# Optimization experiments

Measured on AMD Instinct MI355X. Metric: run time of the kernel, lower is better.

Reference implementation:

```python
import jax, jax.numpy as jnp
import numpy as np


def _patch_indices():
    # 36 positions (6x6 grid), each gathering a 3x3 window of 6-channel squares
    # from the flattened 385-vector: index = x*48 + y*6 + c
    idx = []
    for i in range(36):
        x, y = i // 6, i % 6
        rows = []
        for ox in range(3):
            for oy in range(3):
                base = (x + ox) * 48 + (y + oy) * 6
                rows.extend(range(base, base + 6))
        idx.append(rows)
    return jnp.asarray(np.array(idx, dtype=np.int32))  # [36, 54]


_IDX = _patch_indices()


def _crelu(v):
    return jnp.clip(v, -1.0, 1.0)


def setup_inputs() -> dict:
    key = jax.random.key(0)
    ks = jax.random.split(key, 13)
    B = 131072
    inp = jax.random.normal(ks[0], (B, 385), dtype=jnp.float32)
    s = 0.2  # small init scale
    # sight stack: 54 -> 8 -> 8 -> 1  (stored as [in, out])
    W1 = jax.random.normal(ks[1], (54, 8), jnp.float32) * s
    b1 = jax.random.normal(ks[2], (8,), jnp.float32) * s
    W2 = jax.random.normal(ks[3], (8, 8), jnp.float32) * s
    b2 = jax.random.normal(ks[4], (8,), jnp.float32) * s
    W3 = jax.random.normal(ks[5], (8, 1), jnp.float32) * s
    b3 = jax.random.normal(ks[6], (1,), jnp.float32) * s
    # evaluation stack: 37 -> 16 -> 16 -> 1
    E1 = jax.random.normal(ks[7], (37, 16), jnp.float32) * s
    c1 = jax.random.normal(ks[8], (16,), jnp.float32) * s
    E2 = jax.random.normal(ks[9], (16, 16), jnp.float32) * s
    c2 = jax.random.normal(ks[10], (16,), jnp.float32) * s
    E3 = jax.random.normal(ks[11], (16, 1), jnp.float32) * s
    c3 = jax.random.normal(ks[12], (1,), jnp.float32) * s
    return {"inp": inp, "W1": W1, "b1": b1, "W2": W2, "b2": b2,
            "W3": W3, "b3": b3, "E1": E1, "c1": c1, "E2": E2, "c2": c2,
            "E3": E3, "c3": c3}


def reference(inp, W1, b1, W2, b2, W3, b3, E1, c1, E2, c2, E3, c3):
    # inp: [B, 385]
    patches = inp[:, _IDX]                       # [B, 36, 54] windowed gather
    h = _crelu(jnp.einsum('bpf,fo->bpo', patches, W1) + b1)   # [B, 36, 8]
    h = _crelu(jnp.einsum('bpf,fo->bpo', h, W2) + b2)         # [B, 36, 8]
    v = _crelu(jnp.einsum('bpf,fo->bpo', h, W3) + b3)[..., 0]  # [B, 36]
    vision = jnp.concatenate([v, inp[:, 384:385]], axis=1)    # [B, 37]
    g = _crelu(vision @ E1 + c1)                 # [B, 16]
    g = _crelu(g @ E2 + c2)                      # [B, 16]
    out = _crelu(g @ E3 + c3)                    # [B, 1]
    return out
```

## Files before the change

kernel.cpp:

```cpp
#include <hip/hip_runtime.h>

typedef __attribute__((ext_vector_type(8))) short short8;
typedef __attribute__((ext_vector_type(4))) float float4v;

__device__ __forceinline__ float crelu(float v) {
    return fminf(1.0f, fmaxf(-1.0f, v));
}
__device__ __forceinline__ ushort f2bf(float v) {
    uint u = __float_as_uint(v);
    u += 0x7fffu + ((u >> 16) & 1u);
    return (ushort)(u >> 16);
}

#define ROW 385
#define BT 16
#define BS 388
#define BOARD_ELEMS (BT * BS)
#define BOARD_TOTAL (BOARD_ELEMS + 64)

__global__ __launch_bounds__(256, 6)
void lila_mfma(const float* __restrict__ inp,
               const float* __restrict__ W1, const float* __restrict__ b1,
               const float* __restrict__ W2, const float* __restrict__ b2,
               const float* __restrict__ W3, const float* __restrict__ b3,
               const float* __restrict__ E1, const float* __restrict__ c1,
               const float* __restrict__ E2, const float* __restrict__ c2,
               const float* __restrict__ E3, const float* __restrict__ c3,
               float* __restrict__ out)
{
    __shared__ __align__(16) ushort s_board[BOARD_TOTAL];
    __shared__ __align__(16) ushort s_h[BT * 36 * 8];
    __shared__ float s_vis[BT * 37];
    __shared__ float s_cen[BT];
    __shared__ float s_g1[BT * 17];
    __shared__ float s_g2[BT * 17];

    const int tid  = threadIdx.x;
    const int lane = tid & 63;
    const int wv   = tid >> 6;
    const int quad = lane >> 4;
    const int nn   = tid & 15;
    const int m0   = quad * 8;
    const long long b0 = (long long)blockIdx.x * BT;

    short8 bfr[3];
    #pragma unroll
    for (int r = 0; r < 3; ++r) {
        #pragma unroll
        for (int j = 0; j < 8; ++j) {
            int k = m0 + j;
            float w = (k < 18 && nn < 8) ? W1[(r * 18 + k) * 8 + nn] : 0.0f;
            bfr[r][j] = (short)f2bf(w);
        }
    }
    const float bias1 = (nn < 8) ? b1[nn] : 0.0f;

    #pragma unroll 1
    for (int rr = 0; rr < 4; ++rr) {
        int row = wv * 4 + rr;
        const float* gr = inp + (b0 + row) * ROW;
        ushort* br = s_board + row * BS;
        #pragma unroll
        for (int s = 0; s < 6; ++s)
            br[lane + 64 * s] = f2bf(gr[lane + 64 * s]);
        if (lane == 0) s_cen[row] = gr[384];
        if (lane < 4)  br[384 + lane] = 0;
    }
    if (tid < 64) s_board[BOARD_ELEMS + tid] = 0;
    __syncthreads();

    #pragma unroll 1
    for (int t = wv; t < 36; t += 4) {
        int task = t * 16 + nn;
        uint b = (uint)task / 36u;
        uint p = (uint)task - 36u * b;
        uint x = p / 6u;
        uint y = p - 6u * x;
        const uint* bp = (const uint*)(s_board + b * BS + x * 48 + 6 * y + m0);
        union { uint u[4]; short8 s; } a0, a1, a2;
        #pragma unroll
        for (int q = 0; q < 4; ++q) {
            a0.u[q] = bp[q];
            a1.u[q] = bp[24 + q];
            a2.u[q] = bp[48 + q];
        }
        float4v acc = { bias1, bias1, bias1, bias1 };
        acc = __builtin_amdgcn_mfma_f32_16x16x32_bf16(a0.s, bfr[0], acc, 0, 0, 0);
        acc = __builtin_amdgcn_mfma_f32_16x16x32_bf16(a1.s, bfr[1], acc, 0, 0, 0);
        acc = __builtin_amdgcn_mfma_f32_16x16x32_bf16(a2.s, bfr[2], acc, 0, 0, 0);
        if (nn < 8) {
            #pragma unroll
            for (int i = 0; i < 4; ++i) {
                int trow = t * 16 + quad * 4 + i;
                s_h[trow * 8 + nn] = f2bf(crelu(acc[i]));
            }
        }
    }
    __syncthreads();

    #pragma unroll 1
    for (int task = tid; task < BT * 36; task += 256) {
        uint b = (uint)task / 36u;
        uint p = (uint)task - 36u * b;
        const uint4* hp = (const uint4*)s_h;
        uint4 hv = hp[task];
        float h[8];
        h[0] = __uint_as_float(hv.x << 16);
        h[1] = __uint_as_float(hv.x & 0xffff0000u);
        h[2] = __uint_as_float(hv.y << 16);
        h[3] = __uint_as_float(hv.y & 0xffff0000u);
        h[4] = __uint_as_float(hv.z << 16);
        h[5] = __uint_as_float(hv.z & 0xffff0000u);
        h[6] = __uint_as_float(hv.w << 16);
        h[7] = __uint_as_float(hv.w & 0xffff0000u);

        float a2[8];
        #pragma unroll
        for (int o = 0; o < 8; ++o) a2[o] = b2[o];
        #pragma unroll
        for (int i = 0; i < 8; ++i) {
            #pragma unroll
            for (int o = 0; o < 8; ++o)
                a2[o] = fmaf(h[i], W2[i * 8 + o], a2[o]);
        }
        float v = b3[0];
        #pragma unroll
        for (int i = 0; i < 8; ++i) v = fmaf(crelu(a2[i]), W3[i], v);
        s_vis[b * 37 + p] = crelu(v);
    }
    if (tid < BT) s_vis[tid * 37 + 36] = s_cen[tid];
    __syncthreads();

    {
        int b = tid & 15, o = tid >> 4;
        float a = c1[o];
        #pragma unroll
        for (int f = 0; f < 37; ++f)
            a = fmaf(s_vis[b * 37 + f], E1[f * 16 + o], a);
        s_g1[b * 17 + o] = crelu(a);
    }
    __syncthreads();
    {
        int b = tid & 15, o = tid >> 4;
        float a = c2[o];
        #pragma unroll
        for (int f = 0; f < 16; ++f)
            a = fmaf(s_g1[b * 17 + f], E2[f * 16 + o], a);
        s_g2[b * 17 + o] = crelu(a);
    }
    __syncthreads();
    if (tid < BT) {
        float a = c3[0];
        #pragma unroll
        for (int f = 0; f < 16; ++f)
            a = fmaf(s_g2[tid * 17 + f], E3[f], a);
        out[b0 + tid] = crelu(a);
    }
}

extern "C" void kernel_launch(void* const* d_in, const int* in_sizes, int n_in,
                              void* d_out, int out_size, void* d_ws, size_t ws_size,
                              hipStream_t stream)
{
    const float* inp = (const float*)d_in[0];
    const float* W1  = (const float*)d_in[1];
    const float* b1  = (const float*)d_in[2];
    const float* W2  = (const float*)d_in[3];
    const float* b2  = (const float*)d_in[4];
    const float* W3  = (const float*)d_in[5];
    const float* b3  = (const float*)d_in[6];
    const float* E1  = (const float*)d_in[7];
    const float* c1  = (const float*)d_in[8];
    const float* E2  = (const float*)d_in[9];
    const float* c2  = (const float*)d_in[10];
    const float* E3  = (const float*)d_in[11];
    const float* c3  = (const float*)d_in[12];
    float* out = (float*)d_out;

    int B = in_sizes[0] / ROW;
    int grid = B / BT;
    lila_mfma<<<grid, 256, 0, stream>>>(inp, W1, b1, W2, b2, W3, b3,
                                        E1, c1, E2, c2, E3, c3, out);
}
```

Measured before the change: 315.9 us.

## Make each wavefront process its own four boards without block barriers

Each of the four wavefronts now owns a private LDS slab and handles four boards end to end: loading, MFMA first layer, per-patch MLP, and the evaluation head. All __syncthreads are replaced by compiler memory fences, and the final layer uses cross-lane shuffles instead of a shared-memory pass. Loads are packed as pairs of bf16 into 32-bit stores, and the LDS footprint is reused across stages so launch bounds can request 7 blocks per CU. The risk is correctness: with no wave-level barrier, ordering between lanes relies on the wavefront executing in lockstep, and some cross-lane LDS reuse (vis overlapping board) could race.

```diff
diff --git a/kernel.cpp b/kernel.cpp
--- a/kernel.cpp
+++ b/kernel.cpp
@@ -6,20 +6,21 @@
 __device__ __forceinline__ float crelu(float v) {
     return fminf(1.0f, fmaxf(-1.0f, v));
 }
-__device__ __forceinline__ ushort f2bf(float v) {
+__device__ __forceinline__ uint f2bf_u(float v) {
     uint u = __float_as_uint(v);
     u += 0x7fffu + ((u >> 16) & 1u);
-    return (ushort)(u >> 16);
+    return u >> 16;
 }
+__device__ __forceinline__ ushort f2bf(float v) { return (ushort)f2bf_u(v); }
 
 #define ROW 385
-#define BT 16
-#define BS 388
-#define BOARD_ELEMS (BT * BS)
-#define BOARD_TOTAL (BOARD_ELEMS + 64)
+#define BT  16
+#define BS  388
 
-__global__ __launch_bounds__(256, 6)
-void lila_mfma(const float* __restrict__ inp,
+#define SLAB_BYTES 5440
+
+__global__ __launch_bounds__(256, 7)
+void lila_wave(const float* __restrict__ inp,
                const float* __restrict__ W1, const float* __restrict__ b1,
                const float* __restrict__ W2, const float* __restrict__ b2,
                const float* __restrict__ W3, const float* __restrict__ b3,
@@ -28,20 +29,22 @@
                const float* __restrict__ E3, const float* __restrict__ c3,
                float* __restrict__ out)
 {
-    __shared__ __align__(16) ushort s_board[BOARD_TOTAL];
-    __shared__ __align__(16) ushort s_h[BT * 36 * 8];
-    __shared__ float s_vis[BT * 37];
-    __shared__ float s_cen[BT];
-    __shared__ float s_g1[BT * 17];
-    __shared__ float s_g2[BT * 17];
+    __shared__ __align__(16) char slab_all[4 * SLAB_BYTES];
 
     const int tid  = threadIdx.x;
     const int lane = tid & 63;
     const int wv   = tid >> 6;
     const int quad = lane >> 4;
-    const int nn   = tid & 15;
+    const int nn   = lane & 15;
     const int m0   = quad * 8;
-    const long long b0 = (long long)blockIdx.x * BT;
+
+    char*   slab  = slab_all + wv * SLAB_BYTES;
+    ushort* board = (ushort*)slab;
+    ushort* hbuf  = (ushort*)(slab + 3136);
+    float*  vis   = (float*)slab;
+    float*  g1    = (float*)(slab + 640);
+
+    const long long b0w = (long long)blockIdx.x * BT + wv * 4;
 
     short8 bfr[3];
     #pragma unroll
@@ -55,28 +58,33 @@
     }
     const float bias1 = (nn < 8) ? b1[nn] : 0.0f;
 
-    #pragma unroll 1
-    for (int rr = 0; rr < 4; ++rr) {
-        int row = wv * 4 + rr;
-        const float* gr = inp + (b0 + row) * ROW;
-        ushort* br = s_board + row * BS;
-        #pragma unroll
-        for (int s = 0; s < 6; ++s)
-            br[lane + 64 * s] = f2bf(gr[lane + 64 * s]);
-        if (lane == 0) s_cen[row] = gr[384];
-        if (lane < 4)  br[384 + lane] = 0;
+    const int r   = lane >> 4;
+    const int c16 = lane & 15;
+    const float* gr = inp + (b0w + r) * ROW;
+
+    if (lane < 4) *(unsigned long long*)(board + lane * BS + 384) = 0ULL;
+    if (lane >= 4 && lane < 8)
+        *(unsigned long long*)(slab + 3104 + (lane - 4) * 8) = 0ULL;
+
+    #pragma unroll
+    for (int j = 0; j < 12; ++j) {
+        int e = 2 * (c16 + 16 * j);
+        float f0 = gr[e], f1 = gr[e + 1];
+        uint pk = f2bf_u(f0) | (f2bf_u(f1) << 16);
+        *(uint*)((char*)board + r * 776 + 2 * e) = pk;
     }
-    if (tid < 64) s_board[BOARD_ELEMS + tid] = 0;
-    __syncthreads();
+    const float cen = gr[384];
+
+    asm volatile("" ::: "memory");
 
     #pragma unroll 1
-    for (int t = wv; t < 36; t += 4) {
-        int task = t * 16 + nn;
-        uint b = (uint)task / 36u;
-        uint p = (uint)task - 36u * b;
-        uint x = p / 6u;
-        uint y = p - 6u * x;
-        const uint* bp = (const uint*)(s_board + b * BS + x * 48 + 6 * y + m0);
+    for (int t = 0; t < 9; ++t) {
+        int ltask = t * 16 + nn;
+        uint lb = (uint)ltask / 36u;
+        uint p  = (uint)ltask - 36u * lb;
+        uint x  = p / 6u;
+        uint y  = p - 6u * x;
+        const uint* bp = (const uint*)(board + lb * BS + x * 48 + 6 * y + m0);
         union { uint u[4]; short8 s; } a0, a1, a2;
         #pragma unroll
         for (int q = 0; q < 4; ++q) {
@@ -92,69 +100,69 @@
             #pragma unroll
             for (int i = 0; i < 4; ++i) {
                 int trow = t * 16 + quad * 4 + i;
-                s_h[trow * 8 + nn] = f2bf(crelu(acc[i]));
+                hbuf[trow * 8 + nn] = f2bf(crelu(acc[i]));
             }
         }
     }
-    __syncthreads();
+
+    asm volatile("" ::: "memory");
 
     #pragma unroll 1
-    for (int task = tid; task < BT * 36; task += 256) {
-        uint b = (uint)task / 36u;
-        uint p = (uint)task - 36u * b;
-        const uint4* hp = (const uint4*)s_h;
-        uint4 hv = hp[task];
-        float h[8];
-        h[0] = __uint_as_float(hv.x << 16);
-        h[1] = __uint_as_float(hv.x & 0xffff0000u);
-        h[2] = __uint_as_float(hv.y << 16);
-        h[3] = __uint_as_float(hv.y & 0xffff0000u);
-        h[4] = __uint_as_float(hv.z << 16);
-        h[5] = __uint_as_float(hv.z & 0xffff0000u);
-        h[6] = __uint_as_float(hv.w << 16);
-        h[7] = __uint_as_float(hv.w & 0xffff0000u);
+    for (int it = 0; it < 3; ++it) {
+        int task = lane + it * 64;
+        if (task < 144) {
+            uint lb = (uint)task / 36u;
+            uint p  = (uint)task - 36u * lb;
+            uint4 hv = *(const uint4*)(hbuf + task * 8);
+            float h[8];
+            h[0] = __uint_as_float(hv.x << 16);
+            h[1] = __uint_as_float(hv.x & 0xffff0000u);
+            h[2] = __uint_as_float(hv.y << 16);
+            h[3] = __uint_as_float(hv.y & 0xffff0000u);
+            h[4] = __uint_as_float(hv.z << 16);
+            h[5] = __uint_as_float(hv.z & 0xffff0000u);
+            h[6] = __uint_as_float(hv.w << 16);
+            h[7] = __uint_as_float(hv.w & 0xffff0000u);
 
-        float a2[8];
-        #pragma unroll
-        for (int o = 0; o < 8; ++o) a2[o] = b2[o];
-        #pragma unroll
-        for (int i = 0; i < 8; ++i) {
+            float a2[8];
             #pragma unroll
-            for (int o = 0; o < 8; ++o)
-                a2[o] = fmaf(h[i], W2[i * 8 + o], a2[o]);
+            for (int o = 0; o < 8; ++o) a2[o] = b2[o];
+            #pragma unroll
+            for (int i = 0; i < 8; ++i) {
+                #pragma unroll
+                for (int o = 0; o < 8; ++o)
+                    a2[o] = fmaf(h[i], W2[i * 8 + o], a2[o]);
+            }
+            float v = b3[0];
+            #pragma unroll
+            for (int i = 0; i < 8; ++i) v = fmaf(crelu(a2[i]), W3[i], v);
+            vis[lb * 40 + p] = crelu(v);
         }
-        float v = b3[0];
-        #pragma unroll
-        for (int i = 0; i < 8; ++i) v = fmaf(crelu(a2[i]), W3[i], v);
-        s_vis[b * 37 + p] = crelu(v);
     }
-    if (tid < BT) s_vis[tid * 37 + 36] = s_cen[tid];
-    __syncthreads();
+
+    asm volatile("" ::: "memory");
 
     {
-        int b = tid & 15, o = tid >> 4;
+        const int o = nn;
         float a = c1[o];
         #pragma unroll
-        for (int f = 0; f < 37; ++f)
-            a = fmaf(s_vis[b * 37 + f], E1[f * 16 + o], a);
-        s_g1[b * 17 + o] = crelu(a);
-    }
-    __syncthreads();
-    {
-        int b = tid & 15, o = tid >> 4;
-        float a = c2[o];
+        for (int f = 0; f < 36; ++f)
+            a = fmaf(vis[r * 40 + f], E1[f * 16 + o], a);
+        a = fmaf(cen, E1[36 * 16 + o], a);
+        g1[r * 17 + o] = crelu(a);
+
+        asm volatile("" ::: "memory");
+
+        float a2 = c2[o];
         #pragma unroll
         for (int f = 0; f < 16; ++f)
-            a = fmaf(s_g1[b * 17 + f], E2[f * 16 + o], a);
-        s_g2[b * 17 + o] = crelu(a);
-    }
-    __syncthreads();
-    if (tid < BT) {
-        float a = c3[0];
-        #pragma unroll
-        for (int f = 0; f < 16; ++f)
-            a = fmaf(s_g2[tid * 17 + f], E3[f], a);
-        out[b0 + tid] = crelu(a);
+            a2 = fmaf(g1[r * 17 + f], E2[f * 16 + o], a2);
+        float t = crelu(a2) * E3[o];
+        t += __shfl_xor(t, 1);
+        t += __shfl_xor(t, 2);
+        t += __shfl_xor(t, 4);
+        t += __shfl_xor(t, 8);
+        if (o == 0) out[b0w + r] = crelu(t + c3[0]);
     }
 }
 
@@ -179,6 +187,6 @@
 
     int B = in_sizes[0] / ROW;
     int grid = B / BT;
-    lila_mfma<<<grid, 256, 0, stream>>>(inp, W1, b1, W2, b2, W3, b3,
+    lila_wave<<<grid, 256, 0, stream>>>(inp, W1, b1, W2, b2, W3, b3,
                                         E1, c1, E2, c2, E3, c3, out);
 }
```

New measurement: 300.5 us. 1.05x faster.
